# Optimization experiments

Measured on AMD Instinct MI355X. Metric: run time of the kernel, lower is better.

Reference implementation:

```python
import jax, jax.numpy as jnp
import numpy as np

B, N, D_MODEL, HIDDEN = 4, 1024, 1024, 1024
N_HEAD, D_KEY, D_VALUE = 16, 64, 64


def setup_inputs() -> dict:
    key = jax.random.key(0)
    ks = jax.random.split(key, 12)
    s = 0.02
    return {
        "queries": jax.random.normal(ks[0], (B, N, D_MODEL), jnp.float32),
        "keys": jax.random.normal(ks[1], (B, N, HIDDEN), jnp.float32),
        "values": jax.random.normal(ks[2], (B, N, HIDDEN), jnp.float32),
        "attn_bias": jax.random.normal(ks[3], (B, N_HEAD, N, N), jnp.float32),
        "Wq": jax.random.normal(ks[4], (D_MODEL, D_KEY * N_HEAD), jnp.float32) * s,
        "bq": jnp.zeros((D_KEY * N_HEAD,), jnp.float32),
        "Wk": jax.random.normal(ks[5], (HIDDEN, D_KEY * N_HEAD), jnp.float32) * s,
        "bk": jnp.zeros((D_KEY * N_HEAD,), jnp.float32),
        "Wv": jax.random.normal(ks[6], (HIDDEN, D_VALUE * N_HEAD), jnp.float32) * s,
        "bv": jnp.zeros((D_VALUE * N_HEAD,), jnp.float32),
        "Wo": jax.random.normal(ks[7], (max(D_MODEL, HIDDEN), D_MODEL), jnp.float32) * s,
        "bo": jnp.zeros((D_MODEL,), jnp.float32),
    }


def reference(queries, keys, values, attn_bias, Wq, bq, Wk, bk, Wv, bv, Wo, bo):
    b, n, _ = queries.shape
    # QKV projections, split heads -> [b, h, n, d]
    q = (queries @ Wq + bq).reshape(b, n, N_HEAD, D_KEY).transpose(0, 2, 1, 3)
    k = (keys @ Wk + bk).reshape(b, keys.shape[1], N_HEAD, D_KEY).transpose(0, 2, 1, 3)
    v = (values @ Wv + bv).reshape(b, values.shape[1], N_HEAD, D_VALUE).transpose(0, 2, 1, 3)
    # scaled dot-product attention with additive bias (dropout_rate=0 -> identity)
    scaled_q = q * (D_KEY ** -0.5)
    product = jnp.einsum("bhqd,bhkd->bhqk", scaled_q, k) + attn_bias
    weights = jax.nn.softmax(product, axis=-1)
    ctx = jnp.einsum("bhqk,bhkd->bhqd", weights, v)
    # combine heads -> [b, n, h*d]
    out = ctx.transpose(0, 2, 1, 3).reshape(b, n, N_HEAD * D_VALUE)
    return out @ Wo + bo
```

## Files before the change

kernel.cpp:

```cpp
#include <hip/hip_runtime.h>
#include <hip/hip_bf16.h>
#include <cstdint>
#include <type_traits>


typedef unsigned short u16;
typedef __attribute__((ext_vector_type(8))) short v8bf;
typedef __attribute__((ext_vector_type(4))) float v4f;

#define DEV static __device__ __forceinline__

DEV float b2f(u16 u) { union { uint32_t u; float f; } v; v.u = ((uint32_t)u) << 16; return v.f; }
DEV u16 f2b(float f) {
    union { float f; uint32_t u; } v; v.f = f;
    uint32_t r = v.u + 0x7FFFu + ((v.u >> 16) & 1u);
    return (u16)(r >> 16);
}

__global__ __launch_bounds__(256) void transpose_w(const float* __restrict__ in,
                                                   u16* __restrict__ out) {
    __shared__ float tile[32][33];
    const int tx = threadIdx.x, ty = threadIdx.y;
    const int n0 = blockIdx.x * 32, k0 = blockIdx.y * 32;
#pragma unroll
    for (int i = 0; i < 4; i++)
        tile[ty + i * 8][tx] = in[(size_t)(k0 + ty + i * 8) * 1024 + n0 + tx];
    __syncthreads();
#pragma unroll
    for (int i = 0; i < 4; i++)
        out[(size_t)(n0 + ty + i * 8) * 1024 + k0 + tx] = f2b(tile[tx][ty + i * 8]);
}

__global__ __launch_bounds__(256) void transpose_v(const u16* __restrict__ V,
                                                   u16* __restrict__ VT) {
    __shared__ u16 tile[32][33];
    const int tx = threadIdx.x, ty = threadIdx.y;
    const int n0 = blockIdx.x * 32, d0 = blockIdx.y * 32, bh = blockIdx.z;
    const int b = bh >> 4, h = bh & 15;
#pragma unroll
    for (int i = 0; i < 4; i++)
        tile[ty + i * 8][tx] = V[(size_t)(b * 1024 + n0 + ty + i * 8) * 1024 + h * 64 + d0 + tx];
    __syncthreads();
#pragma unroll
    for (int i = 0; i < 4; i++)
        VT[(size_t)(bh * 64 + d0 + ty + i * 8) * 1024 + n0 + tx] = tile[tx][ty + i * 8];
}

template <typename TA, typename TO>
__global__ __launch_bounds__(256) void gemm_nt(const TA* __restrict__ A,
                                               const u16* __restrict__ Bt,
                                               const float* __restrict__ bias,
                                               TO* __restrict__ C) {
    __shared__ __align__(16) u16 aS[128][72];
    __shared__ __align__(16) u16 bS[128][72];
    const int tid = threadIdx.x;
    const int wave = tid >> 6, lane = tid & 63;
    const int l16 = lane & 15, quad = lane >> 4;
    const int m0 = blockIdx.x * 128, n0 = blockIdx.y * 128;
    const int mb = (wave >> 1) * 64, nb = (wave & 1) * 64;

    v4f acc[4][4];
#pragma unroll
    for (int i = 0; i < 4; i++)
#pragma unroll
        for (int j = 0; j < 4; j++) acc[i][j] = (v4f){0.f, 0.f, 0.f, 0.f};

    for (int kk = 0; kk < 1024; kk += 64) {
        __syncthreads();
        if constexpr (std::is_same_v<TA, float>) {
#pragma unroll
            for (int i = 0; i < 8; i++) {
                const int idx = tid + 256 * i;
                const int row = idx >> 4, c4 = idx & 15;
                const float4 f = *reinterpret_cast<const float4*>(
                    &A[(size_t)(m0 + row) * 1024 + kk + c4 * 4]);
                union { u16 h[4]; uint2 v; } pk;
                pk.h[0] = f2b(f.x); pk.h[1] = f2b(f.y);
                pk.h[2] = f2b(f.z); pk.h[3] = f2b(f.w);
                *reinterpret_cast<uint2*>(&aS[row][c4 * 4]) = pk.v;
            }
        } else {
#pragma unroll
            for (int i = 0; i < 4; i++) {
                const int idx = tid + 256 * i;
                const int row = idx >> 3, off = idx & 7;
                *reinterpret_cast<int4*>(&aS[row][off * 8]) =
                    *reinterpret_cast<const int4*>(&A[(size_t)(m0 + row) * 1024 + kk + off * 8]);
            }
        }
#pragma unroll
        for (int i = 0; i < 4; i++) {
            const int idx = tid + 256 * i;
            const int row = idx >> 3, off = idx & 7;
            *reinterpret_cast<int4*>(&bS[row][off * 8]) =
                *reinterpret_cast<const int4*>(&Bt[(size_t)(n0 + row) * 1024 + kk + off * 8]);
        }
        __syncthreads();
#pragma unroll
        for (int kt = 0; kt < 2; kt++) {
            v8bf af[4], bfr[4];
#pragma unroll
            for (int i = 0; i < 4; i++) {
                af[i]  = *reinterpret_cast<const v8bf*>(&aS[mb + i * 16 + l16][kt * 32 + quad * 8]);
                bfr[i] = *reinterpret_cast<const v8bf*>(&bS[nb + i * 16 + l16][kt * 32 + quad * 8]);
            }
#pragma unroll
            for (int i = 0; i < 4; i++)
#pragma unroll
                for (int j = 0; j < 4; j++)
                    acc[i][j] = __builtin_amdgcn_mfma_f32_16x16x32_bf16(af[i], bfr[j], acc[i][j], 0, 0, 0);
        }
    }
    float bv[4];
#pragma unroll
    for (int j = 0; j < 4; j++) bv[j] = bias[n0 + nb + j * 16 + l16];
#pragma unroll
    for (int i = 0; i < 4; i++)
#pragma unroll
        for (int j = 0; j < 4; j++) {
            const int col = n0 + nb + j * 16 + l16;
#pragma unroll
            for (int r = 0; r < 4; r++) {
                const int row = m0 + mb + i * 16 + quad * 4 + r;
                const float val = acc[i][j][r] + bv[j];
                if constexpr (std::is_same_v<TO, u16>) C[(size_t)row * 1024 + col] = f2b(val);
                else                                   C[(size_t)row * 1024 + col] = val;
            }
        }
}

__global__ __launch_bounds__(256) void attn_kernel(const u16* __restrict__ Q,
                                                   const u16* __restrict__ K,
                                                   const u16* __restrict__ VT,
                                                   const float* __restrict__ bias,
                                                   u16* __restrict__ ctx) {
    __shared__ __align__(16) u16 kS[128][72];
    __shared__ __align__(16) u16 vS[64][136];
    __shared__ __align__(16) u16 pS[4][16][40];
    __shared__ float rsLDS[4][16];
    __shared__ float ctxLDS[4][16][64];

    const int tid = threadIdx.x;
    const int wave = tid >> 6, lane = tid & 63, l16 = lane & 15, quad = lane >> 4;
    const int q0 = blockIdx.x * 16;
    const int bh = blockIdx.y;
    const int b = bh >> 4, h = bh & 15;

    v8bf qf[2];
    {
        const size_t qrow = (size_t)(b * 1024 + q0 + l16) * 1024 + h * 64;
        qf[0] = *reinterpret_cast<const v8bf*>(&Q[qrow + quad * 8]);
        qf[1] = *reinterpret_cast<const v8bf*>(&Q[qrow + 32 + quad * 8]);
    }

    v4f ctxacc[4];
#pragma unroll
    for (int v = 0; v < 4; v++) ctxacc[v] = (v4f){0.f, 0.f, 0.f, 0.f};
    float rs[4] = {0.f, 0.f, 0.f, 0.f};

    const size_t kbase = (size_t)b * 1024 * 1024 + (size_t)h * 64;
    const size_t vtbase = (size_t)bh * 64 * 1024;
    const size_t bbase = ((size_t)bh * 1024 + q0) * 1024;

    for (int c = 0; c < 8; c++) {
        const int nc = c * 128;
        __syncthreads();
#pragma unroll
        for (int i = 0; i < 4; i++) {
            const int idx = tid + 256 * i;
            const int key = idx >> 3, off = idx & 7;
            *reinterpret_cast<int4*>(&kS[key][off * 8]) =
                *reinterpret_cast<const int4*>(&K[kbase + (size_t)(nc + key) * 1024 + off * 8]);
        }
#pragma unroll
        for (int i = 0; i < 4; i++) {
            const int idx = tid + 256 * i;
            const int d = idx >> 4, off = idx & 15;
            *reinterpret_cast<int4*>(&vS[d][off * 8]) =
                *reinterpret_cast<const int4*>(&VT[vtbase + (size_t)d * 1024 + nc + off * 8]);
        }
        __syncthreads();
#pragma unroll
        for (int t = 0; t < 2; t++) {
            v4f s = (v4f){0.f, 0.f, 0.f, 0.f};
#pragma unroll
            for (int kt = 0; kt < 2; kt++) {
                v8bf bfr = *reinterpret_cast<const v8bf*>(&kS[wave * 32 + t * 16 + l16][kt * 32 + quad * 8]);
                s = __builtin_amdgcn_mfma_f32_16x16x32_bf16(qf[kt], bfr, s, 0, 0, 0);
            }
            const int keyg = nc + wave * 32 + t * 16 + l16;
#pragma unroll
            for (int r = 0; r < 4; r++) {
                const float lg = s[r] * 0.125f + bias[bbase + (size_t)(quad * 4 + r) * 1024 + keyg];
                const float p = __expf(lg);
                rs[r] += p;
                pS[wave][quad * 4 + r][t * 16 + l16] = f2b(p);
            }
        }
        __syncthreads();
        {
            v8bf pf = *reinterpret_cast<const v8bf*>(&pS[wave][l16][quad * 8]);
#pragma unroll
            for (int v = 0; v < 4; v++) {
                v8bf vf = *reinterpret_cast<const v8bf*>(&vS[v * 16 + l16][wave * 32 + quad * 8]);
                ctxacc[v] = __builtin_amdgcn_mfma_f32_16x16x32_bf16(pf, vf, ctxacc[v], 0, 0, 0);
            }
        }
    }

#pragma unroll
    for (int r = 0; r < 4; r++) {
        float v = rs[r];
        v += __shfl_xor(v, 1, 16);
        v += __shfl_xor(v, 2, 16);
        v += __shfl_xor(v, 4, 16);
        v += __shfl_xor(v, 8, 16);
        rs[r] = v;
    }
    if (l16 == 0) {
#pragma unroll
        for (int r = 0; r < 4; r++) rsLDS[wave][quad * 4 + r] = rs[r];
    }
#pragma unroll
    for (int v = 0; v < 4; v++)
#pragma unroll
        for (int r = 0; r < 4; r++)
            ctxLDS[wave][quad * 4 + r][v * 16 + l16] = ctxacc[v][r];
    __syncthreads();
#pragma unroll
    for (int i = 0; i < 4; i++) {
        const int row = (tid >> 6) + 4 * i;
        const int d = tid & 63;
        const float sum = ctxLDS[0][row][d] + ctxLDS[1][row][d] + ctxLDS[2][row][d] + ctxLDS[3][row][d];
        const float den = rsLDS[0][row] + rsLDS[1][row] + rsLDS[2][row] + rsLDS[3][row];
        ctx[(size_t)(b * 1024 + q0 + row) * 1024 + h * 64 + d] = f2b(sum / den);
    }
}

extern "C" void kernel_launch(void* const* d_in, const int* in_sizes, int n_in,
                              void* d_out, int out_size, void* d_ws, size_t ws_size,
                              hipStream_t stream) {
    const float* queries = (const float*)d_in[0];
    const float* keys    = (const float*)d_in[1];
    const float* values  = (const float*)d_in[2];
    const float* abias   = (const float*)d_in[3];
    const float* Wq = (const float*)d_in[4];
    const float* bq = (const float*)d_in[5];
    const float* Wk = (const float*)d_in[6];
    const float* bk = (const float*)d_in[7];
    const float* Wv = (const float*)d_in[8];
    const float* bv = (const float*)d_in[9];
    const float* Wo = (const float*)d_in[10];
    const float* bo = (const float*)d_in[11];
    float* out = (float*)d_out;

    char* ws = (char*)d_ws;
    u16* Qb   = (u16*)(ws);
    u16* Kb   = (u16*)(ws + (size_t)(8u << 20));
    u16* Vb   = (u16*)(ws + (size_t)(16u << 20));
    u16* VTb  = (u16*)(ws + (size_t)(24u << 20));
    u16* ctxb = (u16*)(ws + (size_t)(32u << 20));
    u16* WqT  = (u16*)(ws + (size_t)(40u << 20));
    u16* WkT  = (u16*)(ws + (size_t)(42u << 20));
    u16* WvT  = (u16*)(ws + (size_t)(44u << 20));
    u16* WoT  = (u16*)(ws + (size_t)(46u << 20));

    dim3 tb(32, 8);
    transpose_w<<<dim3(32, 32), tb, 0, stream>>>(Wq, WqT);
    transpose_w<<<dim3(32, 32), tb, 0, stream>>>(Wk, WkT);
    transpose_w<<<dim3(32, 32), tb, 0, stream>>>(Wv, WvT);
    transpose_w<<<dim3(32, 32), tb, 0, stream>>>(Wo, WoT);

    gemm_nt<float, u16><<<dim3(32, 8), 256, 0, stream>>>(queries, WqT, bq, Qb);
    gemm_nt<float, u16><<<dim3(32, 8), 256, 0, stream>>>(keys,    WkT, bk, Kb);
    gemm_nt<float, u16><<<dim3(32, 8), 256, 0, stream>>>(values,  WvT, bv, Vb);

    transpose_v<<<dim3(32, 2, 64), tb, 0, stream>>>(Vb, VTb);

    attn_kernel<<<dim3(64, 64), 256, 0, stream>>>(Qb, Kb, VTb, abias, ctxb);

    gemm_nt<u16, float><<<dim3(32, 8), 256, 0, stream>>>(ctxb, WoT, bo, out);
}
```

Before: 586.2 us.

## Rewrite pipeline with direct global-to-LDS loads, fused QKV GEMM and restructured attention

Replaces nearly all kernels. Inputs are pre-cast to bf16, the four weight transposes and three QKV GEMMs are each merged into one batched launch, and the V projection writes its transposed layout directly so the separate transpose kernel is gone. The GEMMs and attention now stage tiles with global_load_lds into XOR-swizzled LDS. The attention kernel handles 64 queries per block, stages the bias tile in LDS, and has each wave own its own query rows, which removes the cross-wave LDS reduction. The softmax scale is folded into the Q projection. This cuts launch count and removes redundant K/V reloads, at the cost of an extra cast pass and more LDS per block.

```diff
diff --git a/kernel.cpp b/kernel.cpp
--- a/kernel.cpp
+++ b/kernel.cpp
@@ -1,5 +1,4 @@
 #include <hip/hip_runtime.h>
-#include <hip/hip_bf16.h>
 #include <cstdint>
 #include <type_traits>
 
@@ -10,16 +9,24 @@
 
 #define DEV static __device__ __forceinline__
 
-DEV float b2f(u16 u) { union { uint32_t u; float f; } v; v.u = ((uint32_t)u) << 16; return v.f; }
 DEV u16 f2b(float f) {
     union { float f; uint32_t u; } v; v.f = f;
     uint32_t r = v.u + 0x7FFFu + ((v.u >> 16) & 1u);
     return (u16)(r >> 16);
 }
 
-__global__ __launch_bounds__(256) void transpose_w(const float* __restrict__ in,
-                                                   u16* __restrict__ out) {
+DEV void gl_lds16(const void* g, void* l) {
+    __builtin_amdgcn_global_load_lds((const __attribute__((address_space(1))) void*)g,
+                                     (__attribute__((address_space(3))) void*)l, 16, 0, 0);
+}
+
+__global__ __launch_bounds__(256) void transpose_w4(const float* __restrict__ w0, const float* __restrict__ w1,
+                                                    const float* __restrict__ w2, const float* __restrict__ w3,
+                                                    u16* __restrict__ o0, u16* __restrict__ o1,
+                                                    u16* __restrict__ o2, u16* __restrict__ o3) {
     __shared__ float tile[32][33];
+    const float* in = blockIdx.z == 0 ? w0 : blockIdx.z == 1 ? w1 : blockIdx.z == 2 ? w2 : w3;
+    u16* out        = blockIdx.z == 0 ? o0 : blockIdx.z == 1 ? o1 : blockIdx.z == 2 ? o2 : o3;
     const int tx = threadIdx.x, ty = threadIdx.y;
     const int n0 = blockIdx.x * 32, k0 = blockIdx.y * 32;
 #pragma unroll
@@ -31,210 +38,231 @@
         out[(size_t)(n0 + ty + i * 8) * 1024 + k0 + tx] = f2b(tile[tx][ty + i * 8]);
 }
 
-__global__ __launch_bounds__(256) void transpose_v(const u16* __restrict__ V,
-                                                   u16* __restrict__ VT) {
-    __shared__ u16 tile[32][33];
-    const int tx = threadIdx.x, ty = threadIdx.y;
-    const int n0 = blockIdx.x * 32, d0 = blockIdx.y * 32, bh = blockIdx.z;
-    const int b = bh >> 4, h = bh & 15;
-#pragma unroll
-    for (int i = 0; i < 4; i++)
-        tile[ty + i * 8][tx] = V[(size_t)(b * 1024 + n0 + ty + i * 8) * 1024 + h * 64 + d0 + tx];
-    __syncthreads();
-#pragma unroll
-    for (int i = 0; i < 4; i++)
-        VT[(size_t)(bh * 64 + d0 + ty + i * 8) * 1024 + n0 + tx] = tile[tx][ty + i * 8];
-}
-
-template <typename TA, typename TO>
-__global__ __launch_bounds__(256) void gemm_nt(const TA* __restrict__ A,
-                                               const u16* __restrict__ Bt,
-                                               const float* __restrict__ bias,
-                                               TO* __restrict__ C) {
-    __shared__ __align__(16) u16 aS[128][72];
-    __shared__ __align__(16) u16 bS[128][72];
-    const int tid = threadIdx.x;
-    const int wave = tid >> 6, lane = tid & 63;
-    const int l16 = lane & 15, quad = lane >> 4;
-    const int m0 = blockIdx.x * 128, n0 = blockIdx.y * 128;
-    const int mb = (wave >> 1) * 64, nb = (wave & 1) * 64;
-
-    v4f acc[4][4];
-#pragma unroll
-    for (int i = 0; i < 4; i++)
-#pragma unroll
-        for (int j = 0; j < 4; j++) acc[i][j] = (v4f){0.f, 0.f, 0.f, 0.f};
-
-    for (int kk = 0; kk < 1024; kk += 64) {
-        __syncthreads();
-        if constexpr (std::is_same_v<TA, float>) {
-#pragma unroll
-            for (int i = 0; i < 8; i++) {
-                const int idx = tid + 256 * i;
-                const int row = idx >> 4, c4 = idx & 15;
-                const float4 f = *reinterpret_cast<const float4*>(
-                    &A[(size_t)(m0 + row) * 1024 + kk + c4 * 4]);
-                union { u16 h[4]; uint2 v; } pk;
-                pk.h[0] = f2b(f.x); pk.h[1] = f2b(f.y);
-                pk.h[2] = f2b(f.z); pk.h[3] = f2b(f.w);
-                *reinterpret_cast<uint2*>(&aS[row][c4 * 4]) = pk.v;
-            }
-        } else {
-#pragma unroll
-            for (int i = 0; i < 4; i++) {
-                const int idx = tid + 256 * i;
-                const int row = idx >> 3, off = idx & 7;
-                *reinterpret_cast<int4*>(&aS[row][off * 8]) =
-                    *reinterpret_cast<const int4*>(&A[(size_t)(m0 + row) * 1024 + kk + off * 8]);
-            }
-        }
-#pragma unroll
-        for (int i = 0; i < 4; i++) {
-            const int idx = tid + 256 * i;
-            const int row = idx >> 3, off = idx & 7;
-            *reinterpret_cast<int4*>(&bS[row][off * 8]) =
-                *reinterpret_cast<const int4*>(&Bt[(size_t)(n0 + row) * 1024 + kk + off * 8]);
-        }
-        __syncthreads();
-#pragma unroll
-        for (int kt = 0; kt < 2; kt++) {
-            v8bf af[4], bfr[4];
-#pragma unroll
-            for (int i = 0; i < 4; i++) {
-                af[i]  = *reinterpret_cast<const v8bf*>(&aS[mb + i * 16 + l16][kt * 32 + quad * 8]);
-                bfr[i] = *reinterpret_cast<const v8bf*>(&bS[nb + i * 16 + l16][kt * 32 + quad * 8]);
-            }
-#pragma unroll
-            for (int i = 0; i < 4; i++)
-#pragma unroll
-                for (int j = 0; j < 4; j++)
-                    acc[i][j] = __builtin_amdgcn_mfma_f32_16x16x32_bf16(af[i], bfr[j], acc[i][j], 0, 0, 0);
-        }
-    }
-    float bv[4];
-#pragma unroll
-    for (int j = 0; j < 4; j++) bv[j] = bias[n0 + nb + j * 16 + l16];
-#pragma unroll
-    for (int i = 0; i < 4; i++)
-#pragma unroll
-        for (int j = 0; j < 4; j++) {
-            const int col = n0 + nb + j * 16 + l16;
-#pragma unroll
-            for (int r = 0; r < 4; r++) {
-                const int row = m0 + mb + i * 16 + quad * 4 + r;
-                const float val = acc[i][j][r] + bv[j];
-                if constexpr (std::is_same_v<TO, u16>) C[(size_t)row * 1024 + col] = f2b(val);
-                else                                   C[(size_t)row * 1024 + col] = val;
-            }
-        }
-}
-
-__global__ __launch_bounds__(256) void attn_kernel(const u16* __restrict__ Q,
-                                                   const u16* __restrict__ K,
-                                                   const u16* __restrict__ VT,
-                                                   const float* __restrict__ bias,
-                                                   u16* __restrict__ ctx) {
-    __shared__ __align__(16) u16 kS[128][72];
-    __shared__ __align__(16) u16 vS[64][136];
-    __shared__ __align__(16) u16 pS[4][16][40];
-    __shared__ float rsLDS[4][16];
-    __shared__ float ctxLDS[4][16][64];
-
+__global__ __launch_bounds__(256) void cast3(const float* __restrict__ a0, const float* __restrict__ a1,
+                                             const float* __restrict__ a2,
+                                             u16* __restrict__ o0, u16* __restrict__ o1, u16* __restrict__ o2) {
+    const int z = blockIdx.y;
+    const float* in = z == 0 ? a0 : z == 1 ? a1 : a2;
+    u16* out        = z == 0 ? o0 : z == 1 ? o1 : o2;
+    const size_t i = ((size_t)blockIdx.x * 256 + threadIdx.x) * 8;
+    const float4 f0 = *reinterpret_cast<const float4*>(in + i);
+    const float4 f1 = *reinterpret_cast<const float4*>(in + i + 4);
+    union { u16 h[8]; uint4 v4; } pk;
+    pk.h[0] = f2b(f0.x); pk.h[1] = f2b(f0.y); pk.h[2] = f2b(f0.z); pk.h[3] = f2b(f0.w);
+    pk.h[4] = f2b(f1.x); pk.h[5] = f2b(f1.y); pk.h[6] = f2b(f1.z); pk.h[7] = f2b(f1.w);
+    *reinterpret_cast<uint4*>(out + i) = pk.v4;
+}
+
+template <int BN, typename TO>
+DEV void gemm_body(const u16* __restrict__ A, const u16* __restrict__ Bt,
+                   const float* __restrict__ bias, TO* __restrict__ C,
+                   u16* __restrict__ Ct, float cscale, bool storeT,
+                   u16* aS, u16* bS) {
+    constexpr int FJ = BN / 32;
     const int tid = threadIdx.x;
     const int wave = tid >> 6, lane = tid & 63, l16 = lane & 15, quad = lane >> 4;
-    const int q0 = blockIdx.x * 16;
-    const int bh = blockIdx.y;
-    const int b = bh >> 4, h = bh & 15;
+    const int m0 = blockIdx.x * 128, n0 = blockIdx.y * BN;
+    const int wr = wave >> 1, wc = wave & 1;
+    const int r8 = lane >> 3, c8 = lane & 7;
+
+    v4f acc[4][FJ];
+#pragma unroll
+    for (int i = 0; i < 4; i++)
+#pragma unroll
+        for (int j = 0; j < FJ; j++) acc[i][j] = (v4f){0.f, 0.f, 0.f, 0.f};
+
+    for (int kk = 0; kk < 1024; kk += 64) {
+        if (kk) __syncthreads();
+#pragma unroll
+        for (int cl = 0; cl < 4; cl++) {
+            const int row = wave * 32 + cl * 8 + r8;
+            gl_lds16(A + (size_t)(m0 + row) * 1024 + kk + ((c8 ^ (row & 7)) * 8),
+                     aS + (wave * 32 + cl * 8) * 64);
+        }
+#pragma unroll
+        for (int cl = 0; cl < BN / 32; cl++) {
+            const int row = wave * (BN / 4) + cl * 8 + r8;
+            gl_lds16(Bt + (size_t)(n0 + row) * 1024 + kk + ((c8 ^ (row & 7)) * 8),
+                     bS + (wave * (BN / 4) + cl * 8) * 64);
+        }
+        __syncthreads();
+#pragma unroll
+        for (int kt = 0; kt < 2; kt++) {
+            v8bf af[4], bf[FJ];
+#pragma unroll
+            for (int i = 0; i < 4; i++) {
+                const int row = wr * 64 + i * 16 + l16;
+                af[i] = *reinterpret_cast<const v8bf*>(aS + row * 64 + (((kt * 4 + quad) ^ (row & 7)) * 8));
+            }
+#pragma unroll
+            for (int j = 0; j < FJ; j++) {
+                const int row = wc * (BN / 2) + j * 16 + l16;
+                bf[j] = *reinterpret_cast<const v8bf*>(bS + row * 64 + (((kt * 4 + quad) ^ (row & 7)) * 8));
+            }
+#pragma unroll
+            for (int i = 0; i < 4; i++)
+#pragma unroll
+                for (int j = 0; j < FJ; j++)
+                    acc[i][j] = __builtin_amdgcn_mfma_f32_16x16x32_bf16(af[i], bf[j], acc[i][j], 0, 0, 0);
+        }
+    }
+    float bv[FJ];
+#pragma unroll
+    for (int j = 0; j < FJ; j++) bv[j] = bias[n0 + wc * (BN / 2) + j * 16 + l16];
+    if (storeT) {
+#pragma unroll
+        for (int i = 0; i < 4; i++)
+#pragma unroll
+            for (int j = 0; j < FJ; j++) {
+                const int col = n0 + wc * (BN / 2) + j * 16 + l16;
+                const int row0 = m0 + wr * 64 + i * 16 + quad * 4;
+                union { u16 h[4]; uint2 u; } pk;
+#pragma unroll
+                for (int r = 0; r < 4; r++) pk.h[r] = f2b((acc[i][j][r] + bv[j]) * cscale);
+                *reinterpret_cast<uint2*>(&Ct[(size_t)col * 4096 + row0]) = pk.u;
+            }
+    } else {
+#pragma unroll
+        for (int i = 0; i < 4; i++)
+#pragma unroll
+            for (int j = 0; j < FJ; j++) {
+                const int col = n0 + wc * (BN / 2) + j * 16 + l16;
+#pragma unroll
+                for (int r = 0; r < 4; r++) {
+                    const int row = m0 + wr * 64 + i * 16 + quad * 4 + r;
+                    const float val = (acc[i][j][r] + bv[j]) * cscale;
+                    if constexpr (std::is_same_v<TO, u16>) C[(size_t)row * 1024 + col] = f2b(val);
+                    else                                   C[(size_t)row * 1024 + col] = val;
+                }
+            }
+    }
+}
+
+__global__ __launch_bounds__(256, 3) void gemm_qkv(
+    const u16* __restrict__ Qc, const u16* __restrict__ Kc, const u16* __restrict__ Vc,
+    const u16* __restrict__ WqT, const u16* __restrict__ WkT, const u16* __restrict__ WvT,
+    const float* __restrict__ bq, const float* __restrict__ bk, const float* __restrict__ bv,
+    u16* __restrict__ Qb, u16* __restrict__ Kb, u16* __restrict__ VT) {
+    __shared__ __align__(16) u16 aS[128 * 64];
+    __shared__ __align__(16) u16 bS[128 * 64];
+    const int z = blockIdx.z;
+    const u16* A    = z == 0 ? Qc : z == 1 ? Kc : Vc;
+    const u16* Bt   = z == 0 ? WqT : z == 1 ? WkT : WvT;
+    const float* bi = z == 0 ? bq : z == 1 ? bk : bv;
+    u16* Cn         = z == 0 ? Qb : Kb;
+    gemm_body<128, u16>(A, Bt, bi, Cn, VT, z == 0 ? 0.125f : 1.0f, z == 2, aS, bS);
+}
+
+__global__ __launch_bounds__(256, 3) void gemm_out(const u16* __restrict__ A, const u16* __restrict__ Bt,
+                                                   const float* __restrict__ bias, float* __restrict__ C) {
+    __shared__ __align__(16) u16 aS[128 * 64];
+    __shared__ __align__(16) u16 bS[64 * 64];
+    gemm_body<64, float>(A, Bt, bias, C, nullptr, 1.0f, false, aS, bS);
+}
+
+__global__ __launch_bounds__(256, 3) void attn2(const u16* __restrict__ Q,
+                                                const u16* __restrict__ K,
+                                                const u16* __restrict__ VT,
+                                                const float* __restrict__ bias,
+                                                u16* __restrict__ ctx) {
+    __shared__ __align__(16) u16 kS[64 * 64];
+    __shared__ __align__(16) u16 vS[64 * 64];
+    __shared__ __align__(16) float biasS[64 * 64];
+    __shared__ __align__(16) u16 pT[4][16 * 72];
+
+    const int tid = threadIdx.x;
+    const int wave = tid >> 6, lane = tid & 63, l16 = lane & 15, quad = lane >> 4;
+    const int q0 = blockIdx.x * 64, bh = blockIdx.y, b = bh >> 4, h = bh & 15;
+    const int r8 = lane >> 3, c8 = lane & 7;
+    const int r16 = lane >> 4, c16 = lane & 15;
 
     v8bf qf[2];
     {
-        const size_t qrow = (size_t)(b * 1024 + q0 + l16) * 1024 + h * 64;
-        qf[0] = *reinterpret_cast<const v8bf*>(&Q[qrow + quad * 8]);
-        qf[1] = *reinterpret_cast<const v8bf*>(&Q[qrow + 32 + quad * 8]);
+        const size_t qrow = ((size_t)(b * 1024 + q0 + wave * 16 + l16)) * 1024 + h * 64;
+        qf[0] = *reinterpret_cast<const v8bf*>(Q + qrow + quad * 8);
+        qf[1] = *reinterpret_cast<const v8bf*>(Q + qrow + 32 + quad * 8);
     }
 
     v4f ctxacc[4];
 #pragma unroll
     for (int v = 0; v < 4; v++) ctxacc[v] = (v4f){0.f, 0.f, 0.f, 0.f};
-    float rs[4] = {0.f, 0.f, 0.f, 0.f};
-
-    const size_t kbase = (size_t)b * 1024 * 1024 + (size_t)h * 64;
-    const size_t vtbase = (size_t)bh * 64 * 1024;
-    const size_t bbase = ((size_t)bh * 1024 + q0) * 1024;
-
-    for (int c = 0; c < 8; c++) {
-        const int nc = c * 128;
+    float rs = 0.f;
+
+    const size_t kg = ((size_t)b * 1024) * 1024 + h * 64;
+    const size_t vg = ((size_t)h * 64) * 4096 + b * 1024;
+    const float* bp = bias + ((size_t)bh * 1024 + q0) * 1024;
+    u16* pw = pT[wave];
+
+    for (int c = 0; c < 16; c++) {
+        const int nc = c * 64;
+        if (c) __syncthreads();
+#pragma unroll
+        for (int cl = 0; cl < 2; cl++) {
+            const int key = wave * 16 + cl * 8 + r8;
+            gl_lds16(K + kg + (size_t)(nc + key) * 1024 + ((c8 ^ (key & 7)) * 8),
+                     kS + (wave * 16 + cl * 8) * 64);
+        }
+#pragma unroll
+        for (int cl = 0; cl < 2; cl++) {
+            const int d = wave * 16 + cl * 8 + r8;
+            gl_lds16(VT + vg + (size_t)d * 4096 + nc + ((c8 ^ (d & 7)) * 8),
+                     vS + (wave * 16 + cl * 8) * 64);
+        }
+#pragma unroll
+        for (int cl = 0; cl < 4; cl++) {
+            const int row = wave * 16 + cl * 4 + r16;
+            gl_lds16(bp + (size_t)row * 1024 + nc + ((c16 ^ (row & 15)) * 4),
+                     biasS + (wave * 16 + cl * 4) * 64);
+        }
         __syncthreads();
-#pragma unroll
-        for (int i = 0; i < 4; i++) {
-            const int idx = tid + 256 * i;
-            const int key = idx >> 3, off = idx & 7;
-            *reinterpret_cast<int4*>(&kS[key][off * 8]) =
-                *reinterpret_cast<const int4*>(&K[kbase + (size_t)(nc + key) * 1024 + off * 8]);
-        }
-#pragma unroll
-        for (int i = 0; i < 4; i++) {
-            const int idx = tid + 256 * i;
-            const int d = idx >> 4, off = idx & 15;
-            *reinterpret_cast<int4*>(&vS[d][off * 8]) =
-                *reinterpret_cast<const int4*>(&VT[vtbase + (size_t)d * 1024 + nc + off * 8]);
-        }
-        __syncthreads();
-#pragma unroll
-        for (int t = 0; t < 2; t++) {
+
+#pragma unroll
+        for (int t = 0; t < 4; t++) {
             v4f s = (v4f){0.f, 0.f, 0.f, 0.f};
 #pragma unroll
             for (int kt = 0; kt < 2; kt++) {
-                v8bf bfr = *reinterpret_cast<const v8bf*>(&kS[wave * 32 + t * 16 + l16][kt * 32 + quad * 8]);
-                s = __builtin_amdgcn_mfma_f32_16x16x32_bf16(qf[kt], bfr, s, 0, 0, 0);
-            }
-            const int keyg = nc + wave * 32 + t * 16 + l16;
-#pragma unroll
-            for (int r = 0; r < 4; r++) {
-                const float lg = s[r] * 0.125f + bias[bbase + (size_t)(quad * 4 + r) * 1024 + keyg];
-                const float p = __expf(lg);
-                rs[r] += p;
-                pS[wave][quad * 4 + r][t * 16 + l16] = f2b(p);
-            }
-        }
-        __syncthreads();
-        {
-            v8bf pf = *reinterpret_cast<const v8bf*>(&pS[wave][l16][quad * 8]);
+                const int krow = t * 16 + l16;
+                const v8bf kf = *reinterpret_cast<const v8bf*>(
+                    kS + krow * 64 + (((kt * 4 + quad) ^ (krow & 7)) * 8));
+                s = __builtin_amdgcn_mfma_f32_16x16x32_bf16(kf, qf[kt], s, 0, 0, 0);
+            }
+            const float4 bi = *reinterpret_cast<const float4*>(
+                biasS + (wave * 16 + l16) * 64 + (((t * 4 + quad) ^ l16) * 4));
+            const float p0 = __expf(s[0] + bi.x);
+            const float p1 = __expf(s[1] + bi.y);
+            const float p2 = __expf(s[2] + bi.z);
+            const float p3 = __expf(s[3] + bi.w);
+            rs += (p0 + p1) + (p2 + p3);
+            union { u16 h[4]; uint2 u; } pk;
+            pk.h[0] = f2b(p0); pk.h[1] = f2b(p1); pk.h[2] = f2b(p2); pk.h[3] = f2b(p3);
+            *reinterpret_cast<uint2*>(pw + l16 * 72 + t * 16 + quad * 4) = pk.u;
+        }
+#pragma unroll
+        for (int kt = 0; kt < 2; kt++) {
+            const v8bf pf = *reinterpret_cast<const v8bf*>(pw + l16 * 72 + kt * 32 + quad * 8);
 #pragma unroll
             for (int v = 0; v < 4; v++) {
-                v8bf vf = *reinterpret_cast<const v8bf*>(&vS[v * 16 + l16][wave * 32 + quad * 8]);
+                const int drow = v * 16 + l16;
+                const v8bf vf = *reinterpret_cast<const v8bf*>(
+                    vS + drow * 64 + (((kt * 4 + quad) ^ (drow & 7)) * 8));
                 ctxacc[v] = __builtin_amdgcn_mfma_f32_16x16x32_bf16(pf, vf, ctxacc[v], 0, 0, 0);
             }
         }
     }
 
-#pragma unroll
-    for (int r = 0; r < 4; r++) {
-        float v = rs[r];
-        v += __shfl_xor(v, 1, 16);
-        v += __shfl_xor(v, 2, 16);
-        v += __shfl_xor(v, 4, 16);
-        v += __shfl_xor(v, 8, 16);
-        rs[r] = v;
-    }
-    if (l16 == 0) {
-#pragma unroll
-        for (int r = 0; r < 4; r++) rsLDS[wave][quad * 4 + r] = rs[r];
-    }
+    rs += __shfl_xor(rs, 16);
+    rs += __shfl_xor(rs, 32);
+    float dninv[4];
+#pragma unroll
+    for (int r = 0; r < 4; r++) dninv[r] = 1.f / __shfl(rs, quad * 4 + r, 16);
 #pragma unroll
     for (int v = 0; v < 4; v++)
 #pragma unroll
-        for (int r = 0; r < 4; r++)
-            ctxLDS[wave][quad * 4 + r][v * 16 + l16] = ctxacc[v][r];
-    __syncthreads();
-#pragma unroll
-    for (int i = 0; i < 4; i++) {
-        const int row = (tid >> 6) + 4 * i;
-        const int d = tid & 63;
-        const float sum = ctxLDS[0][row][d] + ctxLDS[1][row][d] + ctxLDS[2][row][d] + ctxLDS[3][row][d];
-        const float den = rsLDS[0][row] + rsLDS[1][row] + rsLDS[2][row] + rsLDS[3][row];
-        ctx[(size_t)(b * 1024 + q0 + row) * 1024 + h * 64 + d] = f2b(sum / den);
-    }
+        for (int r = 0; r < 4; r++) {
+            const int row = q0 + wave * 16 + quad * 4 + r;
+            ctx[((size_t)(b * 1024 + row)) * 1024 + h * 64 + v * 16 + l16] =
+                f2b(ctxacc[v][r] * dninv[r]);
+        }
 }
 
 extern "C" void kernel_launch(void* const* d_in, const int* in_sizes, int n_in,
@@ -257,27 +285,19 @@
     char* ws = (char*)d_ws;
     u16* Qb   = (u16*)(ws);
     u16* Kb   = (u16*)(ws + (size_t)(8u << 20));
-    u16* Vb   = (u16*)(ws + (size_t)(16u << 20));
-    u16* VTb  = (u16*)(ws + (size_t)(24u << 20));
-    u16* ctxb = (u16*)(ws + (size_t)(32u << 20));
-    u16* WqT  = (u16*)(ws + (size_t)(40u << 20));
-    u16* WkT  = (u16*)(ws + (size_t)(42u << 20));
-    u16* WvT  = (u16*)(ws + (size_t)(44u << 20));
-    u16* WoT  = (u16*)(ws + (size_t)(46u << 20));
-
-    dim3 tb(32, 8);
-    transpose_w<<<dim3(32, 32), tb, 0, stream>>>(Wq, WqT);
-    transpose_w<<<dim3(32, 32), tb, 0, stream>>>(Wk, WkT);
-    transpose_w<<<dim3(32, 32), tb, 0, stream>>>(Wv, WvT);
-    transpose_w<<<dim3(32, 32), tb, 0, stream>>>(Wo, WoT);
-
-    gemm_nt<float, u16><<<dim3(32, 8), 256, 0, stream>>>(queries, WqT, bq, Qb);
-    gemm_nt<float, u16><<<dim3(32, 8), 256, 0, stream>>>(keys,    WkT, bk, Kb);
-    gemm_nt<float, u16><<<dim3(32, 8), 256, 0, stream>>>(values,  WvT, bv, Vb);
-
-    transpose_v<<<dim3(32, 2, 64), tb, 0, stream>>>(Vb, VTb);
-
-    attn_kernel<<<dim3(64, 64), 256, 0, stream>>>(Qb, Kb, VTb, abias, ctxb);
-
-    gemm_nt<u16, float><<<dim3(32, 8), 256, 0, stream>>>(ctxb, WoT, bo, out);
-}
+    u16* VTb  = (u16*)(ws + (size_t)(16u << 20));
+    u16* ctxb = (u16*)(ws + (size_t)(24u << 20));
+    u16* Qc   = (u16*)(ws + (size_t)(32u << 20));
+    u16* Kc   = (u16*)(ws + (size_t)(40u << 20));
+    u16* Vc   = (u16*)(ws + (size_t)(48u << 20));
+    u16* WqT  = (u16*)(ws + (size_t)(56u << 20));
+    u16* WkT  = (u16*)(ws + (size_t)(58u << 20));
+    u16* WvT  = (u16*)(ws + (size_t)(60u << 20));
+    u16* WoT  = (u16*)(ws + (size_t)(62u << 20));
+
+    transpose_w4<<<dim3(32, 32, 4), dim3(32, 8), 0, stream>>>(Wq, Wk, Wv, Wo, WqT, WkT, WvT, WoT);
+    cast3<<<dim3(2048, 3), 256, 0, stream>>>(queries, keys, values, Qc, Kc, Vc);
+    gemm_qkv<<<dim3(32, 8, 3), 256, 0, stream>>>(Qc, Kc, Vc, WqT, WkT, WvT, bq, bk, bv, Qb, Kb, VTb);
+    attn2<<<dim3(16, 64), 256, 0, stream>>>(Qb, Kb, VTb, abias, ctxb);
+    gemm_out<<<dim3(32, 16), 256, 0, stream>>>(ctxb, WoT, bo, out);
+}
```

New measurement: 491.0 us. 16.2% less time.
